# Performance work log

Hardware: AMD Instinct MI355X
Metric: run time of the kernel (lower is better)

## Reference

```python
import jax, jax.numpy as jnp
import numpy as np

B, L, DIM, DFF = 4, 2048, 1024, 4096
EPS = 1e-5

def setup_inputs() -> dict:
    key = jax.random.key(0)
    ks = jax.random.split(key, 10)
    s = 0.02
    return {
        "x": jax.random.normal(ks[0], (B, L, DIM), dtype=jnp.float32),
        "ln_g": jnp.ones((DIM,), jnp.float32),
        "ln_b": jnp.zeros((DIM,), jnp.float32),
        "phazor": jax.random.normal(ks[1], (DIM, 2), dtype=jnp.float32),
        "phazor_init": jax.random.normal(ks[2], (DIM, 2), dtype=jnp.float32),
        "w1": jax.random.normal(ks[3], (DIM, DFF), dtype=jnp.float32) * s,
        "b1": jnp.zeros((DFF,), jnp.float32),
        "w2": jax.random.normal(ks[4], (DFF, DIM), dtype=jnp.float32) * s,
        "b2": jnp.zeros((DIM,), jnp.float32),
        "last_conv_re": jax.random.normal(ks[5], (B, DIM), dtype=jnp.float32),
        "last_conv_im": jax.random.normal(ks[6], (B, DIM), dtype=jnp.float32),
    }

def layer_norm(x, g, b):
    mu = jnp.mean(x, axis=-1, keepdims=True)
    var = jnp.var(x, axis=-1, keepdims=True)
    return (x - mu) * jax.lax.rsqrt(var + EPS) * g + b

def spiral_conv(x, phazor, phazor_init, last_re, last_im):
    # x: [B, L, D] float32
    Lx = x.shape[1]
    p = jax.lax.complex(phazor[:, 0], phazor[:, 1])          # [D]
    p_init = jax.lax.complex(phazor_init[:, 0], phazor_init[:, 1])
    pa = jnp.abs(p)
    p = p / pa * jnp.exp(-pa)                                 # normalized decay phazor
    t = jnp.arange(Lx)
    prog = p[None, :] ** t[:, None]                           # [L, D] p^t
    filt = prog * p_init[None, :]                             # [L, D]
    ffilt = jnp.fft.fft(filt, n=2 * Lx, axis=0)               # [2L, D]
    xf = jnp.fft.fft(x.astype(jnp.complex64), n=2 * Lx, axis=1)  # [B, 2L, D]
    conv = jnp.fft.ifft(ffilt[None] * xf, axis=1)[:, :Lx]     # [B, L, D]
    last = jax.lax.complex(last_re, last_im)                  # [B, D] (detached state)
    conv_with_past = conv + last[:, None, :] * prog[None] * p[None, None, :]
    return conv_with_past.real

def reference(x, ln_g, ln_b, phazor, phazor_init, w1, b1, w2, b2, last_conv_re, last_conv_im):
    x_ = x
    h = layer_norm(x, ln_g, ln_b)
    h = spiral_conv(h, phazor, phazor_init, last_conv_re, last_conv_im)
    x = h + x_
    x_ = x
    h = layer_norm(x, ln_g, ln_b)  # same LayerNorm params reused, as in the source
    h = jax.nn.silu(h @ w1 + b1) @ w2 + b2  # FFN, dropout=0 (eval)
    return h + x_

if __name__ == "__main__":
    out = reference(**setup_inputs())
    print(out.shape, out.dtype)
```

## Files before the change

kernel.cpp:

```cpp
#include <hip/hip_runtime.h>
#include <stdint.h>
#include <stddef.h>

#define DIMC 1024
#define LSEQ 2048
#define BSZ  4
#define DFFC 4096
#define NTOK (BSZ*LSEQ)
#define NCHUNK 32
#define CHUNK 64

typedef __bf16 bf16x8 __attribute__((ext_vector_type(8)));
typedef float  f32x4  __attribute__((ext_vector_type(4)));

__device__ __forceinline__ unsigned short f2bf(float f) {
  unsigned int u = __float_as_uint(f);
  u += 0x7fffu + ((u >> 16) & 1u);
  return (unsigned short)(u >> 16);
}

__device__ __forceinline__ void async16(const void* g, void* l) {
  __builtin_amdgcn_global_load_lds(
      (const __attribute__((address_space(1))) unsigned int*)(uintptr_t)g,
      (__attribute__((address_space(3))) unsigned int*)(uintptr_t)l,
      16, 0, 0);
}

__device__ __forceinline__ void bar() {
  asm volatile("" ::: "memory");
  __builtin_amdgcn_s_barrier();
  asm volatile("" ::: "memory");
}
#define VMCNT(n) asm volatile("s_waitcnt vmcnt(" #n ")" ::: "memory")
#define MFMA_BF16 __builtin_amdgcn_mfma_f32_16x16x32_bf16

__global__ __launch_bounds__(256) void ln_stats(const float* __restrict__ x,
                                                float* __restrict__ mu,
                                                float* __restrict__ rstd) {
  const int token = blockIdx.x;
  const float4* xp = (const float4*)(x + (size_t)token * DIMC);
  float4 v = xp[threadIdx.x];
  float s  = v.x + v.y + v.z + v.w;
  float s2 = v.x*v.x + v.y*v.y + v.z*v.z + v.w*v.w;
  #pragma unroll
  for (int o = 32; o; o >>= 1) { s += __shfl_down(s, o); s2 += __shfl_down(s2, o); }
  __shared__ float sh[8];
  const int lane = threadIdx.x & 63, w = threadIdx.x >> 6;
  if (lane == 0) { sh[w] = s; sh[4 + w] = s2; }
  __syncthreads();
  if (threadIdx.x == 0) {
    float ts  = sh[0] + sh[1] + sh[2] + sh[3];
    float ts2 = sh[4] + sh[5] + sh[6] + sh[7];
    float m = ts * (1.f / DIMC);
    float var = ts2 * (1.f / DIMC) - m * m;
    mu[token] = m;
    rstd[token] = rsqrtf(var + 1e-5f);
  }
}

__global__ __launch_bounds__(256) void ln_fused_bf16(const float* __restrict__ x,
                                                     const float* __restrict__ g,
                                                     const float* __restrict__ bb,
                                                     unsigned short* __restrict__ out) {
  const int token = blockIdx.x;
  const float4* xp = (const float4*)(x + (size_t)token * DIMC);
  float4 v = xp[threadIdx.x];
  float s  = v.x + v.y + v.z + v.w;
  float s2 = v.x*v.x + v.y*v.y + v.z*v.z + v.w*v.w;
  #pragma unroll
  for (int o = 32; o; o >>= 1) { s += __shfl_down(s, o); s2 += __shfl_down(s2, o); }
  __shared__ float sh[10];
  const int lane = threadIdx.x & 63, w = threadIdx.x >> 6;
  if (lane == 0) { sh[w] = s; sh[4 + w] = s2; }
  __syncthreads();
  if (threadIdx.x == 0) {
    float ts  = sh[0] + sh[1] + sh[2] + sh[3];
    float ts2 = sh[4] + sh[5] + sh[6] + sh[7];
    float m = ts * (1.f / DIMC);
    float var = ts2 * (1.f / DIMC) - m * m;
    sh[8] = m;
    sh[9] = rsqrtf(var + 1e-5f);
  }
  __syncthreads();
  const float m = sh[8], r = sh[9];
  float4 gv = ((const float4*)g)[threadIdx.x];
  float4 bv = ((const float4*)bb)[threadIdx.x];
  ushort4 o;
  o.x = f2bf((v.x - m) * r * gv.x + bv.x);
  o.y = f2bf((v.y - m) * r * gv.y + bv.y);
  o.z = f2bf((v.z - m) * r * gv.z + bv.z);
  o.w = f2bf((v.w - m) * r * gv.w + bv.w);
  ((ushort4*)(out + (size_t)token * DIMC))[threadIdx.x] = o;
}

__global__ __launch_bounds__(256) void transpose_bf16(const float* __restrict__ w,
                                                      unsigned short* __restrict__ wt,
                                                      int K, int N) {
  __shared__ float tile[32][33];
  const int n0 = blockIdx.x * 32, k0 = blockIdx.y * 32;
  const int tx = threadIdx.x, ty = threadIdx.y;
  #pragma unroll
  for (int i = 0; i < 32; i += 8)
    tile[ty + i][tx] = w[(size_t)(k0 + ty + i) * N + n0 + tx];
  __syncthreads();
  #pragma unroll
  for (int i = 0; i < 32; i += 8)
    wt[(size_t)(n0 + ty + i) * K + k0 + tx] = f2bf(tile[tx][ty + i]);
}

__device__ __forceinline__ void get_p(const float* __restrict__ phazor, int d,
                                      float& p_re, float& p_im) {
  float pre = phazor[2 * d], pim = phazor[2 * d + 1];
  float a = sqrtf(pre * pre + pim * pim);
  float sc = expf(-a) / a;
  p_re = pre * sc;
  p_im = pim * sc;
}

__global__ __launch_bounds__(256) void scan_phase1(const float* __restrict__ x,
                                                   const float* __restrict__ mu,
                                                   const float* __restrict__ rstd,
                                                   const float* __restrict__ g,
                                                   const float* __restrict__ bb,
                                                   const float* __restrict__ phazor,
                                                   float* __restrict__ Sre,
                                                   float* __restrict__ Sim) {
  const int d = blockIdx.x * 256 + threadIdx.x;
  const int c = blockIdx.y;
  const int b = blockIdx.z;
  float p_re, p_im; get_p(phazor, d, p_re, p_im);
  const float gd = g[d], bd = bb[d];
  const int t0 = c * CHUNK;
  const float* xp  = x + ((size_t)(b * LSEQ + t0)) * DIMC + d;
  const float* mup = mu + b * LSEQ + t0;
  const float* rp  = rstd + b * LSEQ + t0;
  float r_re = 0.f, r_im = 0.f;
  #pragma unroll 4
  for (int s = 0; s < CHUNK; ++s) {
    float hv = (xp[(size_t)s * DIMC] - mup[s]) * rp[s] * gd + bd;
    float nr = p_re * r_re - p_im * r_im + hv;
    float ni = p_re * r_im + p_im * r_re;
    r_re = nr; r_im = ni;
  }
  const int bd_i = b * DIMC + d;
  Sre[c * (BSZ * DIMC) + bd_i] = r_re;
  Sim[c * (BSZ * DIMC) + bd_i] = r_im;
}

__global__ __launch_bounds__(256) void scan_phase2(const float* __restrict__ phazor,
                                                   const float* __restrict__ Sre,
                                                   const float* __restrict__ Sim,
                                                   float* __restrict__ Cre,
                                                   float* __restrict__ Cim) {
  const int bd = blockIdx.x * 256 + threadIdx.x;
  const int d = bd & (DIMC - 1);
  float p_re, p_im; get_p(phazor, d, p_re, p_im);
  float br = p_re, bi = p_im;
  #pragma unroll
  for (int i = 0; i < 6; ++i) { float t = br * br - bi * bi; bi = 2.f * br * bi; br = t; }
  float R_re = 0.f, R_im = 0.f;
  for (int c = 0; c < NCHUNK; ++c) {
    Cre[c * (BSZ * DIMC) + bd] = R_re;
    Cim[c * (BSZ * DIMC) + bd] = R_im;
    float sre = Sre[c * (BSZ * DIMC) + bd], sim = Sim[c * (BSZ * DIMC) + bd];
    float nr = br * R_re - bi * R_im + sre;
    float ni = br * R_im + bi * R_re + sim;
    R_re = nr; R_im = ni;
  }
}

__global__ __launch_bounds__(256) void scan_phase3(const float* __restrict__ x,
                                                   const float* __restrict__ mu,
                                                   const float* __restrict__ rstd,
                                                   const float* __restrict__ g,
                                                   const float* __restrict__ bb,
                                                   const float* __restrict__ phazor,
                                                   const float* __restrict__ phazor_init,
                                                   const float* __restrict__ last_re,
                                                   const float* __restrict__ last_im,
                                                   const float* __restrict__ Cre,
                                                   const float* __restrict__ Cim,
                                                   float* __restrict__ x2) {
  const int d = blockIdx.x * 256 + threadIdx.x;
  const int c = blockIdx.y;
  const int b = blockIdx.z;
  float p_re, p_im; get_p(phazor, d, p_re, p_im);
  const float pi_re = phazor_init[2 * d], pi_im = phazor_init[2 * d + 1];
  const float gd = g[d], bd_ = bb[d];
  const int bd_i = b * DIMC + d;
  float r_re = Cre[c * (BSZ * DIMC) + bd_i];
  float r_im = Cim[c * (BSZ * DIMC) + bd_i];
  float br = p_re, bi = p_im;
  #pragma unroll
  for (int i = 0; i < 6; ++i) { float t = br * br - bi * bi; bi = 2.f * br * bi; br = t; }
  float er = 1.f, ei = 0.f;
  int e = c;
  while (e) {
    if (e & 1) { float t = er * br - ei * bi; ei = er * bi + ei * br; er = t; }
    float t2 = br * br - bi * bi; bi = 2.f * br * bi; br = t2;
    e >>= 1;
  }
  const float lre = last_re[bd_i], lim = last_im[bd_i];
  float q_re = lre * er - lim * ei;
  float q_im = lre * ei + lim * er;
  const int t0 = c * CHUNK;
  const float* xp  = x + ((size_t)(b * LSEQ + t0)) * DIMC + d;
  const float* mup = mu + b * LSEQ + t0;
  const float* rp  = rstd + b * LSEQ + t0;
  float* op = x2 + ((size_t)(b * LSEQ + t0)) * DIMC + d;
  #pragma unroll 4
  for (int s = 0; s < CHUNK; ++s) {
    float xv = xp[(size_t)s * DIMC];
    float hv = (xv - mup[s]) * rp[s] * gd + bd_;
    float nr = p_re * r_re - p_im * r_im + hv;
    float ni = p_re * r_im + p_im * r_re;
    r_re = nr; r_im = ni;
    float nq = p_re * q_re - p_im * q_im;
    q_im = p_re * q_im + p_im * q_re;
    q_re = nq;
    op[(size_t)s * DIMC] = pi_re * r_re - pi_im * r_im + q_re + xv;
  }
}

template<int BN, int EPI>
__global__ __launch_bounds__(512, 2) void gemm8(const unsigned short* __restrict__ A,
                                                const unsigned short* __restrict__ Bt,
                                                const float* __restrict__ bias,
                                                const float* __restrict__ resid,
                                                void* __restrict__ outp,
                                                int M, int N, int K) {
  constexpr int AUS = 256 * 32;
  constexpr int BUS = BN * 32;
  constexpr int BUFUS = 2 * AUS + 2 * BUS;
  constexpr int MI = (BN == 256) ? 8 : 4;
  constexpr int LDSUS = (2 * BUFUS > 65536) ? 2 * BUFUS : 65536;
  __shared__ __align__(16) unsigned short lds[LDSUS];

  const int tid  = threadIdx.x;
  const int lane = tid & 63;
  const int wave = tid >> 6;
  const int wm = (BN == 256) ? (wave & 1) * 128 : (wave >> 1) * 64;
  const int wn = (BN == 256) ? (wave >> 1) * 64  : (wave & 1) * 64;
  const int r15 = lane & 15;
  const int cus = ((lane >> 4) ^ ((r15 >> 1) & 3)) * 8;

  int bid = blockIdx.x;
  const int cpx = gridDim.x >> 3;
  bid = (bid & 7) * cpx + (bid >> 3);
  const int ntn = N / BN;
  const int tm = (bid / ntn) * 256;
  const int tn = (bid % ntn) * BN;
  const int NT = K >> 6;

  f32x4 acc[MI][4];
  #pragma unroll
  for (int i = 0; i < MI; ++i)
    #pragma unroll
    for (int j = 0; j < 4; ++j) acc[i][j] = (f32x4){0.f, 0.f, 0.f, 0.f};

  auto stageA = [&](int buf, int kk, int k0) {
    unsigned short* blk = lds + buf * BUFUS + kk * AUS;
    const unsigned short* g = A + (size_t)tm * K + k0 + kk * 32;
    #pragma unroll
    for (int r = 0; r < 2; ++r) {
      const int s = r * 512 + tid;
      const int row = s >> 2;
      const int cg = (s & 3) ^ ((s >> 3) & 3);
      async16(g + (size_t)row * K + cg * 8, blk + (size_t)s * 8);
    }
  };
  auto stageB = [&](int buf, int kk, int k0) {
    unsigned short* blk = lds + buf * BUFUS + 2 * AUS + kk * BUS;
    const unsigned short* g = Bt + (size_t)tn * K + k0 + kk * 32;
    #pragma unroll
    for (int r = 0; r < BN / 128; ++r) {
      const int s = r * 512 + tid;
      const int row = s >> 2;
      const int cg = (s & 3) ^ ((s >> 3) & 3);
      async16(g + (size_t)row * K + cg * 8, blk + (size_t)s * 8);
    }
  };
  auto rdA = [&](int buf, int kk, int mi) -> bf16x8 {
    return *(const bf16x8*)(lds + buf * BUFUS + kk * AUS + (wm + mi * 16 + r15) * 32 + cus);
  };
  auto rdB = [&](int buf, int kk, int ni) -> bf16x8 {
    return *(const bf16x8*)(lds + buf * BUFUS + 2 * AUS + kk * BUS + (wn + ni * 16 + r15) * 32 + cus);
  };

  bf16x8 af[MI], bq0, bq1, bq2, bq3;

  stageA(0, 0, 0); stageB(0, 0, 0); stageA(0, 1, 0); stageB(0, 1, 0);
  if constexpr (BN == 256) VMCNT(4); else VMCNT(3);
  bar();

  for (int t = 0; t < NT - 1; ++t) {
    const int buf = t & 1, nb = buf ^ 1, kn = (t + 1) << 6;
    #pragma unroll
    for (int mi = 0; mi < MI; ++mi) af[mi] = rdA(buf, 0, mi);
    bq0 = rdB(buf, 0, 0); bq1 = rdB(buf, 0, 1);
    stageA(nb, 0, kn);
    bar();
    __builtin_amdgcn_s_setprio(1);
    #pragma unroll
    for (int mi = 0; mi < MI; ++mi) {
      acc[mi][0] = MFMA_BF16(af[mi], bq0, acc[mi][0], 0, 0, 0);
      acc[mi][1] = MFMA_BF16(af[mi], bq1, acc[mi][1], 0, 0, 0);
    }
    __builtin_amdgcn_s_setprio(0);
    bar();
    bq2 = rdB(buf, 0, 2); bq3 = rdB(buf, 0, 3);
    stageB(nb, 0, kn);
    bar();
    __builtin_amdgcn_s_setprio(1);
    #pragma unroll
    for (int mi = 0; mi < MI; ++mi) {
      acc[mi][2] = MFMA_BF16(af[mi], bq2, acc[mi][2], 0, 0, 0);
      acc[mi][3] = MFMA_BF16(af[mi], bq3, acc[mi][3], 0, 0, 0);
    }
    __builtin_amdgcn_s_setprio(0);
    if constexpr (BN == 256) VMCNT(4); else VMCNT(3);
    bar();
    #pragma unroll
    for (int mi = 0; mi < MI; ++mi) af[mi] = rdA(buf, 1, mi);
    bq0 = rdB(buf, 1, 0); bq1 = rdB(buf, 1, 1);
    stageA(nb, 1, kn);
    bar();
    __builtin_amdgcn_s_setprio(1);
    #pragma unroll
    for (int mi = 0; mi < MI; ++mi) {
      acc[mi][0] = MFMA_BF16(af[mi], bq0, acc[mi][0], 0, 0, 0);
      acc[mi][1] = MFMA_BF16(af[mi], bq1, acc[mi][1], 0, 0, 0);
    }
    __builtin_amdgcn_s_setprio(0);
    bar();
    bq2 = rdB(buf, 1, 2); bq3 = rdB(buf, 1, 3);
    stageB(nb, 1, kn);
    bar();
    __builtin_amdgcn_s_setprio(1);
    #pragma unroll
    for (int mi = 0; mi < MI; ++mi) {
      acc[mi][2] = MFMA_BF16(af[mi], bq2, acc[mi][2], 0, 0, 0);
      acc[mi][3] = MFMA_BF16(af[mi], bq3, acc[mi][3], 0, 0, 0);
    }
    __builtin_amdgcn_s_setprio(0);
    if constexpr (BN == 256) VMCNT(4); else VMCNT(3);
    bar();
  }

  {
    const int buf = (NT - 1) & 1;
    #pragma unroll
    for (int mi = 0; mi < MI; ++mi) af[mi] = rdA(buf, 0, mi);
    bq0 = rdB(buf, 0, 0); bq1 = rdB(buf, 0, 1);
    bar();
    #pragma unroll
    for (int mi = 0; mi < MI; ++mi) {
      acc[mi][0] = MFMA_BF16(af[mi], bq0, acc[mi][0], 0, 0, 0);
      acc[mi][1] = MFMA_BF16(af[mi], bq1, acc[mi][1], 0, 0, 0);
    }
    bar();
    bq2 = rdB(buf, 0, 2); bq3 = rdB(buf, 0, 3);
    #pragma unroll
    for (int mi = 0; mi < MI; ++mi) {
      acc[mi][2] = MFMA_BF16(af[mi], bq2, acc[mi][2], 0, 0, 0);
      acc[mi][3] = MFMA_BF16(af[mi], bq3, acc[mi][3], 0, 0, 0);
    }
    VMCNT(0);
    bar();
    #pragma unroll
    for (int mi = 0; mi < MI; ++mi) af[mi] = rdA(buf, 1, mi);
    bq0 = rdB(buf, 1, 0); bq1 = rdB(buf, 1, 1);
    bar();
    #pragma unroll
    for (int mi = 0; mi < MI; ++mi) {
      acc[mi][0] = MFMA_BF16(af[mi], bq0, acc[mi][0], 0, 0, 0);
      acc[mi][1] = MFMA_BF16(af[mi], bq1, acc[mi][1], 0, 0, 0);
    }
    bar();
    bq2 = rdB(buf, 1, 2); bq3 = rdB(buf, 1, 3);
    #pragma unroll
    for (int mi = 0; mi < MI; ++mi) {
      acc[mi][2] = MFMA_BF16(af[mi], bq2, acc[mi][2], 0, 0, 0);
      acc[mi][3] = MFMA_BF16(af[mi], bq3, acc[mi][3], 0, 0, 0);
    }
  }

  const int rg = (lane >> 4) * 4;
  float bias_r[4];
  #pragma unroll
  for (int ni = 0; ni < 4; ++ni) bias_r[ni] = bias[tn + wn + ni * 16 + r15];

  bar();
  if constexpr (EPI == 0) {
    unsigned short* C = lds;
    #pragma unroll
    for (int mi = 0; mi < MI; ++mi)
      #pragma unroll
      for (int ni = 0; ni < 4; ++ni) {
        const int c0 = wn + ni * 16 + r15;
        #pragma unroll
        for (int j = 0; j < 4; ++j) {
          const int r = wm + mi * 16 + rg + j;
          const int key = (((r & 3) ^ ((r >> 2) & 3)) << 4);
          float v = acc[mi][ni][j] + bias_r[ni];
          v = v / (1.f + __expf(-v));
          C[r * 256 + (c0 ^ key)] = f2bf(v);
        }
      }
    bar();
    #pragma unroll
    for (int i = 0; i < 16; ++i) {
      const int off = i * 4096 + tid * 8;
      const int r = off >> 8;
      const int pc = off & 255;
      const int key = (((r & 3) ^ ((r >> 2) & 3)) << 4);
      bf16x8 v = *(const bf16x8*)(C + off);
      *(bf16x8*)((unsigned short*)outp + (size_t)(tm + r) * N + tn + (pc ^ key)) = v;
    }
  } else {
    float* C = (float*)lds;
    #pragma unroll
    for (int mi = 0; mi < MI; ++mi)
      #pragma unroll
      for (int ni = 0; ni < 4; ++ni) {
        const int c0 = wn + ni * 16 + r15;
        #pragma unroll
        for (int j = 0; j < 4; ++j) {
          const int r = wm + mi * 16 + rg + j;
          const int key = (((r & 3) ^ ((r >> 2) & 3)) << 4);
          C[r * 128 + (c0 ^ key)] = acc[mi][ni][j] + bias_r[ni];
        }
      }
    bar();
    #pragma unroll
    for (int i = 0; i < 16; ++i) {
      const int off = i * 2048 + tid * 4;
      const int r = off >> 7;
      const int pc = off & 127;
      const int key = (((r & 3) ^ ((r >> 2) & 3)) << 4);
      f32x4 v = *(const f32x4*)(C + off);
      const size_t gaddr = (size_t)(tm + r) * N + tn + (pc ^ key);
      f32x4 rv = *(const f32x4*)(resid + gaddr);
      v += rv;
      *(f32x4*)((float*)outp + gaddr) = v;
    }
  }
}

extern "C" void kernel_launch(void* const* d_in, const int* in_sizes, int n_in,
                              void* d_out, int out_size, void* d_ws, size_t ws_size,
                              hipStream_t stream) {
  const float* x           = (const float*)d_in[0];
  const float* ln_g        = (const float*)d_in[1];
  const float* ln_b        = (const float*)d_in[2];
  const float* phazor      = (const float*)d_in[3];
  const float* phazor_init = (const float*)d_in[4];
  const float* w1          = (const float*)d_in[5];
  const float* b1          = (const float*)d_in[6];
  const float* w2          = (const float*)d_in[7];
  const float* b2          = (const float*)d_in[8];
  const float* last_re     = (const float*)d_in[9];
  const float* last_im     = (const float*)d_in[10];
  float* out = (float*)d_out;
  char* ws = (char*)d_ws;
  const size_t MB = 1ull << 20;

  float* x2  = (float*)(ws);
  float* mu1 = (float*)(ws + 32 * MB);
  float* rs1 = (float*)(ws + 32 * MB + 64 * 1024);
  float* Sre = (float*)(ws + 32 * MB + 256 * 1024);
  float* Sim = (float*)(ws + 32 * MB + 768 * 1024);
  float* Cre = (float*)(ws + 32 * MB + 1280 * 1024);
  float* Cim = (float*)(ws + 32 * MB + 1792 * 1024);
  unsigned short* h2  = (unsigned short*)(ws + 35 * MB);
  unsigned short* hid = (unsigned short*)(ws + 51 * MB);
  unsigned short* w1t = (unsigned short*)(ws + 115 * MB);
  unsigned short* w2t = (unsigned short*)(ws + 123 * MB);

  transpose_bf16<<<dim3(DFFC / 32, DIMC / 32), dim3(32, 8), 0, stream>>>(w1, w1t, DIMC, DFFC);
  transpose_bf16<<<dim3(DIMC / 32, DFFC / 32), dim3(32, 8), 0, stream>>>(w2, w2t, DFFC, DIMC);

  ln_stats<<<NTOK, 256, 0, stream>>>(x, mu1, rs1);
  scan_phase1<<<dim3(DIMC / 256, NCHUNK, BSZ), 256, 0, stream>>>(x, mu1, rs1, ln_g, ln_b, phazor, Sre, Sim);
  scan_phase2<<<(BSZ * DIMC) / 256, 256, 0, stream>>>(phazor, Sre, Sim, Cre, Cim);
  scan_phase3<<<dim3(DIMC / 256, NCHUNK, BSZ), 256, 0, stream>>>(x, mu1, rs1, ln_g, ln_b, phazor,
                                                                 phazor_init, last_re, last_im,
                                                                 Cre, Cim, x2);
  ln_fused_bf16<<<NTOK, 256, 0, stream>>>(x2, ln_g, ln_b, h2);

  gemm8<256, 0><<<(NTOK / 256) * (DFFC / 256), 512, 0, stream>>>(h2, w1t, b1, nullptr, hid,
                                                                 NTOK, DFFC, DIMC);
  gemm8<128, 1><<<(NTOK / 256) * (DIMC / 128), 512, 0, stream>>>(hid, w2t, b2, x2, out,
                                                                 NTOK, DIMC, DFFC);
}
```

Measured before the change: 329.1 us.

## Deepen GEMM pipeline to three stages and batch scan loads

```diff
diff --git a/kernel.cpp b/kernel.cpp
--- a/kernel.cpp
+++ b/kernel.cpp
@@ -31,7 +31,16 @@
   __builtin_amdgcn_s_barrier();
   asm volatile("" ::: "memory");
 }
+#define LGKM0 do { asm volatile("s_waitcnt lgkmcnt(0)" ::: "memory"); \
+                   __builtin_amdgcn_sched_barrier(0); } while (0)
 #define VMCNT(n) asm volatile("s_waitcnt vmcnt(" #n ")" ::: "memory")
+template <int N> __device__ __forceinline__ void vmwait() {
+  if constexpr (N == 0) VMCNT(0);
+  else if constexpr (N == 3) VMCNT(3);
+  else if constexpr (N == 4) VMCNT(4);
+  else if constexpr (N == 6) VMCNT(6);
+  else if constexpr (N == 8) VMCNT(8);
+}
 #define MFMA_BF16 __builtin_amdgcn_mfma_f32_16x16x32_bf16
 
 __global__ __launch_bounds__(256) void ln_stats(const float* __restrict__ x,
@@ -135,12 +144,18 @@
   const float* mup = mu + b * LSEQ + t0;
   const float* rp  = rstd + b * LSEQ + t0;
   float r_re = 0.f, r_im = 0.f;
-  #pragma unroll 4
-  for (int s = 0; s < CHUNK; ++s) {
-    float hv = (xp[(size_t)s * DIMC] - mup[s]) * rp[s] * gd + bd;
-    float nr = p_re * r_re - p_im * r_im + hv;
-    float ni = p_re * r_im + p_im * r_re;
-    r_re = nr; r_im = ni;
+  #pragma unroll
+  for (int s8 = 0; s8 < CHUNK; s8 += 8) {
+    float xv[8];
+    #pragma unroll
+    for (int k = 0; k < 8; ++k) xv[k] = xp[(size_t)(s8 + k) * DIMC];
+    #pragma unroll
+    for (int k = 0; k < 8; ++k) {
+      float hv = (xv[k] - mup[s8 + k]) * rp[s8 + k] * gd + bd;
+      float nr = p_re * r_re - p_im * r_im + hv;
+      float ni = p_re * r_im + p_im * r_re;
+      r_re = nr; r_im = ni;
+    }
   }
   const int bd_i = b * DIMC + d;
   Sre[c * (BSZ * DIMC) + bd_i] = r_re;
@@ -158,13 +173,19 @@
   float br = p_re, bi = p_im;
   #pragma unroll
   for (int i = 0; i < 6; ++i) { float t = br * br - bi * bi; bi = 2.f * br * bi; br = t; }
+  float sre[NCHUNK], sim[NCHUNK];
+  #pragma unroll
+  for (int c = 0; c < NCHUNK; ++c) {
+    sre[c] = Sre[c * (BSZ * DIMC) + bd];
+    sim[c] = Sim[c * (BSZ * DIMC) + bd];
+  }
   float R_re = 0.f, R_im = 0.f;
+  #pragma unroll
   for (int c = 0; c < NCHUNK; ++c) {
     Cre[c * (BSZ * DIMC) + bd] = R_re;
     Cim[c * (BSZ * DIMC) + bd] = R_im;
-    float sre = Sre[c * (BSZ * DIMC) + bd], sim = Sim[c * (BSZ * DIMC) + bd];
-    float nr = br * R_re - bi * R_im + sre;
-    float ni = br * R_im + bi * R_re + sim;
+    float nr = br * R_re - bi * R_im + sre[c];
+    float ni = br * R_im + bi * R_re + sim[c];
     R_re = nr; R_im = ni;
   }
 }
@@ -208,17 +229,22 @@
   const float* mup = mu + b * LSEQ + t0;
   const float* rp  = rstd + b * LSEQ + t0;
   float* op = x2 + ((size_t)(b * LSEQ + t0)) * DIMC + d;
-  #pragma unroll 4
-  for (int s = 0; s < CHUNK; ++s) {
-    float xv = xp[(size_t)s * DIMC];
-    float hv = (xv - mup[s]) * rp[s] * gd + bd_;
-    float nr = p_re * r_re - p_im * r_im + hv;
-    float ni = p_re * r_im + p_im * r_re;
-    r_re = nr; r_im = ni;
-    float nq = p_re * q_re - p_im * q_im;
-    q_im = p_re * q_im + p_im * q_re;
-    q_re = nq;
-    op[(size_t)s * DIMC] = pi_re * r_re - pi_im * r_im + q_re + xv;
+  #pragma unroll
+  for (int s8 = 0; s8 < CHUNK; s8 += 8) {
+    float xv[8];
+    #pragma unroll
+    for (int k = 0; k < 8; ++k) xv[k] = xp[(size_t)(s8 + k) * DIMC];
+    #pragma unroll
+    for (int k = 0; k < 8; ++k) {
+      float hv = (xv[k] - mup[s8 + k]) * rp[s8 + k] * gd + bd_;
+      float nr = p_re * r_re - p_im * r_im + hv;
+      float ni = p_re * r_im + p_im * r_re;
+      r_re = nr; r_im = ni;
+      float nq = p_re * q_re - p_im * q_im;
+      q_im = p_re * q_im + p_im * q_re;
+      q_re = nq;
+      op[(size_t)(s8 + k) * DIMC] = pi_re * r_re - pi_im * r_im + q_re + xv[k];
+    }
   }
 }
 
@@ -232,15 +258,15 @@
   constexpr int AUS = 256 * 32;
   constexpr int BUS = BN * 32;
   constexpr int BUFUS = 2 * AUS + 2 * BUS;
-  constexpr int MI = (BN == 256) ? 8 : 4;
+  constexpr int NI = (BN == 256) ? 4 : 2;
   constexpr int LDSUS = (2 * BUFUS > 65536) ? 2 * BUFUS : 65536;
   __shared__ __align__(16) unsigned short lds[LDSUS];
 
   const int tid  = threadIdx.x;
   const int lane = tid & 63;
   const int wave = tid >> 6;
-  const int wm = (BN == 256) ? (wave & 1) * 128 : (wave >> 1) * 64;
-  const int wn = (BN == 256) ? (wave >> 1) * 64  : (wave & 1) * 64;
+  const int wm = (wave & 1) * 128;
+  const int wn = (wave >> 1) * (BN / 4);
   const int r15 = lane & 15;
   const int cus = ((lane >> 4) ^ ((r15 >> 1) & 3)) * 8;
 
@@ -252,33 +278,30 @@
   const int tn = (bid % ntn) * BN;
   const int NT = K >> 6;
 
-  f32x4 acc[MI][4];
-  #pragma unroll
-  for (int i = 0; i < MI; ++i)
-    #pragma unroll
-    for (int j = 0; j < 4; ++j) acc[i][j] = (f32x4){0.f, 0.f, 0.f, 0.f};
-
-  auto stageA = [&](int buf, int kk, int k0) {
+  f32x4 acc[8][NI];
+  #pragma unroll
+  for (int i = 0; i < 8; ++i)
+    #pragma unroll
+    for (int j = 0; j < NI; ++j) acc[i][j] = (f32x4){0.f, 0.f, 0.f, 0.f};
+
+  auto stageA1 = [&](int buf, int kk, int k0, int half) {
     unsigned short* blk = lds + buf * BUFUS + kk * AUS;
     const unsigned short* g = A + (size_t)tm * K + k0 + kk * 32;
-    #pragma unroll
-    for (int r = 0; r < 2; ++r) {
-      const int s = r * 512 + tid;
-      const int row = s >> 2;
-      const int cg = (s & 3) ^ ((s >> 3) & 3);
-      async16(g + (size_t)row * K + cg * 8, blk + (size_t)s * 8);
-    }
+    const int s = half * 512 + tid;
+    const int row = s >> 2;
+    const int cg = (s & 3) ^ ((s >> 3) & 3);
+    async16(g + (size_t)row * K + cg * 8, blk + (size_t)s * 8);
   };
-  auto stageB = [&](int buf, int kk, int k0) {
+  auto stageB1 = [&](int buf, int kk, int k0, int half) {
     unsigned short* blk = lds + buf * BUFUS + 2 * AUS + kk * BUS;
     const unsigned short* g = Bt + (size_t)tn * K + k0 + kk * 32;
-    #pragma unroll
-    for (int r = 0; r < BN / 128; ++r) {
-      const int s = r * 512 + tid;
-      const int row = s >> 2;
-      const int cg = (s & 3) ^ ((s >> 3) & 3);
-      async16(g + (size_t)row * K + cg * 8, blk + (size_t)s * 8);
-    }
+    const int s = half * 512 + tid;
+    const int row = s >> 2;
+    const int cg = (s & 3) ^ ((s >> 3) & 3);
+    async16(g + (size_t)row * K + cg * 8, blk + (size_t)s * 8);
+  };
+  auto stageBb = [&](int buf, int kk, int k0) {
+    if constexpr (BN == 256) stageB1(buf, kk, k0, 1);
   };
   auto rdA = [&](int buf, int kk, int mi) -> bf16x8 {
     return *(const bf16x8*)(lds + buf * BUFUS + kk * AUS + (wm + mi * 16 + r15) * 32 + cus);
@@ -287,116 +310,74 @@
     return *(const bf16x8*)(lds + buf * BUFUS + 2 * AUS + kk * BUS + (wn + ni * 16 + r15) * 32 + cus);
   };
 
-  bf16x8 af[MI], bq0, bq1, bq2, bq3;
-
-  stageA(0, 0, 0); stageB(0, 0, 0); stageA(0, 1, 0); stageB(0, 1, 0);
-  if constexpr (BN == 256) VMCNT(4); else VMCNT(3);
+  bf16x8 af[4], bq[NI];
+  constexpr int VMS = (BN == 256) ? 8 : 6;
+  constexpr int VMP = (BN == 256) ? 4 : 3;
+
+#define PH(buf, kk, mh, BREAD, WAIT, ...)                                       \
+  {                                                                             \
+    _Pragma("unroll")                                                           \
+    for (int q = 0; q < 4; ++q) af[q] = rdA(buf, kk, (mh) * 4 + q);             \
+    if (BREAD) {                                                                \
+      _Pragma("unroll")                                                         \
+      for (int n = 0; n < NI; ++n) bq[n] = rdB(buf, kk, n);                     \
+    }                                                                           \
+    __VA_ARGS__;                                                                \
+    bar(); LGKM0;                                                               \
+    __builtin_amdgcn_s_setprio(1);                                              \
+    _Pragma("unroll")                                                           \
+    for (int q = 0; q < 4; ++q)                                                 \
+      _Pragma("unroll")                                                         \
+      for (int n = 0; n < NI; ++n)                                              \
+        acc[(mh) * 4 + q][n] = MFMA_BF16(af[q], bq[n], acc[(mh) * 4 + q][n], 0, 0, 0); \
+    __builtin_amdgcn_s_setprio(0);                                              \
+    WAIT;                                                                       \
+    bar();                                                                      \
+  }
+
+  stageA1(0, 0, 0, 0); stageA1(0, 0, 0, 1); stageB1(0, 0, 0, 0); stageBb(0, 0, 0);
+  stageA1(0, 1, 0, 0); stageA1(0, 1, 0, 1); stageB1(0, 1, 0, 0); stageBb(0, 1, 0);
+  stageA1(1, 0, 64, 0); stageA1(1, 0, 64, 1); stageB1(1, 0, 64, 0); stageBb(1, 0, 64);
+  vmwait<VMS>();
   bar();
 
-  for (int t = 0; t < NT - 1; ++t) {
-    const int buf = t & 1, nb = buf ^ 1, kn = (t + 1) << 6;
-    #pragma unroll
-    for (int mi = 0; mi < MI; ++mi) af[mi] = rdA(buf, 0, mi);
-    bq0 = rdB(buf, 0, 0); bq1 = rdB(buf, 0, 1);
-    stageA(nb, 0, kn);
-    bar();
-    __builtin_amdgcn_s_setprio(1);
-    #pragma unroll
-    for (int mi = 0; mi < MI; ++mi) {
-      acc[mi][0] = MFMA_BF16(af[mi], bq0, acc[mi][0], 0, 0, 0);
-      acc[mi][1] = MFMA_BF16(af[mi], bq1, acc[mi][1], 0, 0, 0);
-    }
-    __builtin_amdgcn_s_setprio(0);
-    bar();
-    bq2 = rdB(buf, 0, 2); bq3 = rdB(buf, 0, 3);
-    stageB(nb, 0, kn);
-    bar();
-    __builtin_amdgcn_s_setprio(1);
-    #pragma unroll
-    for (int mi = 0; mi < MI; ++mi) {
-      acc[mi][2] = MFMA_BF16(af[mi], bq2, acc[mi][2], 0, 0, 0);
-      acc[mi][3] = MFMA_BF16(af[mi], bq3, acc[mi][3], 0, 0, 0);
-    }
-    __builtin_amdgcn_s_setprio(0);
-    if constexpr (BN == 256) VMCNT(4); else VMCNT(3);
-    bar();
-    #pragma unroll
-    for (int mi = 0; mi < MI; ++mi) af[mi] = rdA(buf, 1, mi);
-    bq0 = rdB(buf, 1, 0); bq1 = rdB(buf, 1, 1);
-    stageA(nb, 1, kn);
-    bar();
-    __builtin_amdgcn_s_setprio(1);
-    #pragma unroll
-    for (int mi = 0; mi < MI; ++mi) {
-      acc[mi][0] = MFMA_BF16(af[mi], bq0, acc[mi][0], 0, 0, 0);
-      acc[mi][1] = MFMA_BF16(af[mi], bq1, acc[mi][1], 0, 0, 0);
-    }
-    __builtin_amdgcn_s_setprio(0);
-    bar();
-    bq2 = rdB(buf, 1, 2); bq3 = rdB(buf, 1, 3);
-    stageB(nb, 1, kn);
-    bar();
-    __builtin_amdgcn_s_setprio(1);
-    #pragma unroll
-    for (int mi = 0; mi < MI; ++mi) {
-      acc[mi][2] = MFMA_BF16(af[mi], bq2, acc[mi][2], 0, 0, 0);
-      acc[mi][3] = MFMA_BF16(af[mi], bq3, acc[mi][3], 0, 0, 0);
-    }
-    __builtin_amdgcn_s_setprio(0);
-    if constexpr (BN == 256) VMCNT(4); else VMCNT(3);
-    bar();
+  for (int i = 0; i < NT / 2 - 1; ++i) {
+    const int kb = (2 * i + 1) * 64, kc = kb + 64, kd = kc + 64;
+    PH(0, 0, 0, 1, ((void)0),    stageA1(1, 1, kb, 0); stageA1(1, 1, kb, 1))
+    PH(0, 0, 1, 0, vmwait<VMS>(), stageB1(1, 1, kb, 0); stageBb(1, 1, kb))
+    PH(0, 1, 0, 1, ((void)0),    stageA1(0, 0, kc, 0); stageA1(0, 0, kc, 1))
+    PH(0, 1, 1, 0, vmwait<VMS>(), stageB1(0, 0, kc, 0); stageBb(0, 0, kc))
+    PH(1, 0, 0, 1, ((void)0),    stageA1(0, 1, kc, 0); stageA1(0, 1, kc, 1))
+    PH(1, 0, 1, 0, vmwait<VMS>(), stageB1(0, 1, kc, 0); stageBb(0, 1, kc))
+    PH(1, 1, 0, 1, ((void)0),    stageA1(1, 0, kd, 0); stageA1(1, 0, kd, 1))
+    PH(1, 1, 1, 0, vmwait<VMS>(), stageB1(1, 0, kd, 0); stageBb(1, 0, kd))
   }
 
   {
-    const int buf = (NT - 1) & 1;
-    #pragma unroll
-    for (int mi = 0; mi < MI; ++mi) af[mi] = rdA(buf, 0, mi);
-    bq0 = rdB(buf, 0, 0); bq1 = rdB(buf, 0, 1);
-    bar();
-    #pragma unroll
-    for (int mi = 0; mi < MI; ++mi) {
-      acc[mi][0] = MFMA_BF16(af[mi], bq0, acc[mi][0], 0, 0, 0);
-      acc[mi][1] = MFMA_BF16(af[mi], bq1, acc[mi][1], 0, 0, 0);
-    }
-    bar();
-    bq2 = rdB(buf, 0, 2); bq3 = rdB(buf, 0, 3);
-    #pragma unroll
-    for (int mi = 0; mi < MI; ++mi) {
-      acc[mi][2] = MFMA_BF16(af[mi], bq2, acc[mi][2], 0, 0, 0);
-      acc[mi][3] = MFMA_BF16(af[mi], bq3, acc[mi][3], 0, 0, 0);
-    }
-    VMCNT(0);
-    bar();
-    #pragma unroll
-    for (int mi = 0; mi < MI; ++mi) af[mi] = rdA(buf, 1, mi);
-    bq0 = rdB(buf, 1, 0); bq1 = rdB(buf, 1, 1);
-    bar();
-    #pragma unroll
-    for (int mi = 0; mi < MI; ++mi) {
-      acc[mi][0] = MFMA_BF16(af[mi], bq0, acc[mi][0], 0, 0, 0);
-      acc[mi][1] = MFMA_BF16(af[mi], bq1, acc[mi][1], 0, 0, 0);
-    }
-    bar();
-    bq2 = rdB(buf, 1, 2); bq3 = rdB(buf, 1, 3);
-    #pragma unroll
-    for (int mi = 0; mi < MI; ++mi) {
-      acc[mi][2] = MFMA_BF16(af[mi], bq2, acc[mi][2], 0, 0, 0);
-      acc[mi][3] = MFMA_BF16(af[mi], bq3, acc[mi][3], 0, 0, 0);
-    }
-  }
+    const int kb = (NT - 1) * 64;
+    PH(0, 0, 0, 1, ((void)0),    stageA1(1, 1, kb, 0); stageA1(1, 1, kb, 1))
+    PH(0, 0, 1, 0, vmwait<VMS>(), stageB1(1, 1, kb, 0); stageBb(1, 1, kb))
+    PH(0, 1, 0, 1, ((void)0),    ((void)0))
+    PH(0, 1, 1, 0, vmwait<VMP>(), ((void)0))
+    PH(1, 0, 0, 1, ((void)0),    ((void)0))
+    PH(1, 0, 1, 0, vmwait<0>(),  ((void)0))
+    PH(1, 1, 0, 1, ((void)0),    ((void)0))
+    PH(1, 1, 1, 0, ((void)0),    ((void)0))
+  }
+#undef PH
 
   const int rg = (lane >> 4) * 4;
-  float bias_r[4];
-  #pragma unroll
-  for (int ni = 0; ni < 4; ++ni) bias_r[ni] = bias[tn + wn + ni * 16 + r15];
+  float bias_r[NI];
+  #pragma unroll
+  for (int ni = 0; ni < NI; ++ni) bias_r[ni] = bias[tn + wn + ni * 16 + r15];
 
   bar();
   if constexpr (EPI == 0) {
     unsigned short* C = lds;
     #pragma unroll
-    for (int mi = 0; mi < MI; ++mi)
+    for (int mi = 0; mi < 8; ++mi)
       #pragma unroll
-      for (int ni = 0; ni < 4; ++ni) {
+      for (int ni = 0; ni < NI; ++ni) {
         const int c0 = wn + ni * 16 + r15;
         #pragma unroll
         for (int j = 0; j < 4; ++j) {
@@ -420,9 +401,9 @@
   } else {
     float* C = (float*)lds;
     #pragma unroll
-    for (int mi = 0; mi < MI; ++mi)
+    for (int mi = 0; mi < 8; ++mi)
       #pragma unroll
-      for (int ni = 0; ni < 4; ++ni) {
+      for (int ni = 0; ni < NI; ++ni) {
         const int c0 = wn + ni * 16 + r15;
         #pragma unroll
         for (int j = 0; j < 4; ++j) {
```

Result: no change. 325.4 us (-1.1%).
